# Kernel optimization log

Measured on AMD Instinct MI355X. Metric: run time of the kernel, lower is better.

Reference implementation:

```python
import jax, jax.numpy as jnp
import numpy as np

BATCH = 4096
TEMP = 0.5
WORLD = 1
B = BATCH * WORLD
N = 2 * B
DIM = 128


def _neg_indices():
    # mask_correlated_samples: ones(N,N) with diagonal and the two +/-B
    # off-diagonals zeroed; negatives are entries where mask is True.
    mask = np.ones((N, N), dtype=bool)
    np.fill_diagonal(mask, False)
    idx = np.arange(B)
    mask[idx, idx + B] = False
    mask[idx + B, idx] = False
    rows, cols = np.nonzero(mask)  # each row has exactly N-2 negatives
    return rows.reshape(N, N - 2), cols.reshape(N, N - 2)

_NEG_ROWS, _NEG_COLS = _neg_indices()


def setup_inputs() -> dict:
    key = jax.random.key(0)
    k1, k2 = jax.random.split(key)
    z_i = jax.random.normal(k1, (BATCH, DIM), dtype=jnp.float32)
    z_j = jax.random.normal(k2, (BATCH, DIM), dtype=jnp.float32)
    return {"z_i": z_i, "z_j": z_j}


def reference(z_i, z_j):
    z = jnp.concatenate([z_i, z_j], axis=0)                 # [N, D]
    z = z / jnp.linalg.norm(z, axis=1, keepdims=True)       # L2 normalize
    # cosine similarity of unit vectors == dot product
    sim = (z @ z.T) / TEMP                                   # [N, N]
    sim_i_j = jnp.diagonal(sim, offset=B)                    # [B]
    sim_j_i = jnp.diagonal(sim, offset=-B)                   # [B]
    pos = jnp.concatenate([sim_i_j, sim_j_i])[:, None]       # [N, 1]
    neg = sim[_NEG_ROWS, _NEG_COLS]                          # [N, N-2]
    logits = jnp.concatenate([pos, neg], axis=1)             # [N, N-1]
    # CrossEntropyLoss(reduction='sum') with labels all zero, then / N
    loss = jnp.sum(jax.scipy.special.logsumexp(logits, axis=1) - logits[:, 0])
    return loss / N
```

## Files before the change

kernel.cpp:

```cpp
#include <hip/hip_runtime.h>
#include <hip/hip_bf16.h>


#define NN 8192
#define BHALF 4096
#define DIMK 128

typedef __bf16 bf16x8 __attribute__((ext_vector_type(8)));
typedef float f32x4 __attribute__((ext_vector_type(4)));

#define C1F 2.8853900817779268f
#define SCALEF 1.6986436f

__global__ __launch_bounds__(256) void nt_normalize(
    const float* __restrict__ zi, const float* __restrict__ zj,
    unsigned int* __restrict__ zb_packed) {
  int row = blockIdx.x * 4 + (threadIdx.x >> 6);
  int lane = threadIdx.x & 63;
  const float* src = (row < BHALF) ? (zi + (size_t)row * DIMK)
                                   : (zj + (size_t)(row - BHALF) * DIMK);
  float2 v = ((const float2*)src)[lane];
  float ss = v.x * v.x + v.y * v.y;
#pragma unroll
  for (int off = 32; off >= 1; off >>= 1) ss += __shfl_xor(ss, off, 64);
  float rn = rsqrtf(ss) * SCALEF;
  __hip_bfloat16 h0 = __float2bfloat16(v.x * rn);
  __hip_bfloat16 h1 = __float2bfloat16(v.y * rn);
  unsigned int packed = ((unsigned int)(*(unsigned short*)&h1) << 16) |
                        (*(unsigned short*)&h0);
  int tile = row >> 4, t = row & 15;
  int cq = lane >> 2;
  int c = cq >> 2, quad = cq & 3;
  size_t widx = ((size_t)((tile * 4 + c) * 64 + quad * 16 + t)) * 4 + (lane & 3);
  zb_packed[widx] = packed;
}

__global__ __launch_bounds__(256, 2) void nt_sim(
    const uint4* __restrict__ zbv, float* __restrict__ part) {
  const int lane = threadIdx.x & 63;
  const int wave = threadIdx.x >> 6;
  const int quad = lane >> 4;
  const int t = lane & 15;
  const int row_tile0 = blockIdx.y * 16 + wave * 4;
  const int TB0 = blockIdx.x * 32;

  bf16x8 A[4][4];
#pragma unroll
  for (int rt = 0; rt < 4; ++rt)
#pragma unroll
    for (int c = 0; c < 4; ++c)
      A[rt][c] = __builtin_bit_cast(
          bf16x8, zbv[(size_t)((row_tile0 + rt) * 4 + c) * 64 + lane]);

  float sum[4][4];
#pragma unroll
  for (int rt = 0; rt < 4; ++rt)
#pragma unroll
    for (int r = 0; r < 4; ++r) sum[rt][r] = 0.f;

  uint4 nb[4];
#pragma unroll
  for (int c = 0; c < 4; ++c) nb[c] = zbv[(size_t)(TB0 * 4 + c) * 64 + lane];

  for (int ct = 0; ct < 32; ++ct) {
    uint4 cb[4];
#pragma unroll
    for (int c = 0; c < 4; ++c) cb[c] = nb[c];
#pragma unroll
    for (int c = 0; c < 4; ++c)
      nb[c] = zbv[(size_t)((TB0 + ct + 1) * 4 + c) * 64 + lane];
    f32x4 acc[4];
#pragma unroll
    for (int rt = 0; rt < 4; ++rt) acc[rt] = (f32x4){0.f, 0.f, 0.f, 0.f};
#pragma unroll
    for (int c = 0; c < 4; ++c)
#pragma unroll
      for (int rt = 0; rt < 4; ++rt)
        acc[rt] = __builtin_amdgcn_mfma_f32_16x16x32_bf16(
            A[rt][c], __builtin_bit_cast(bf16x8, cb[c]), acc[rt], 0, 0, 0);
#pragma unroll
    for (int rt = 0; rt < 4; ++rt)
#pragma unroll
      for (int r = 0; r < 4; ++r)
        sum[rt][r] += __builtin_amdgcn_exp2f(acc[rt][r]);
  }

#pragma unroll
  for (int off = 8; off >= 1; off >>= 1)
#pragma unroll
    for (int rt = 0; rt < 4; ++rt)
#pragma unroll
      for (int r = 0; r < 4; ++r)
        sum[rt][r] += __shfl_xor(sum[rt][r], off, 16);

  if (t == 0) {
    float* dst = part + (size_t)blockIdx.x * NN;
    int row_base = row_tile0 * 16;
#pragma unroll
    for (int rt = 0; rt < 4; ++rt)
#pragma unroll
      for (int r = 0; r < 4; ++r)
        dst[row_base + rt * 16 + quad * 4 + r] = sum[rt][r];
  }
}

__device__ __forceinline__ float bf2f(unsigned short s) {
  unsigned int u = (unsigned int)s << 16;
  return __builtin_bit_cast(float, u);
}

__global__ __launch_bounds__(256) void nt_finalize(
    const uint4* __restrict__ zbv, const float* __restrict__ part,
    float* __restrict__ out) {
  int i = blockIdx.x * 256 + threadIdx.x;
  int tile = i >> 4, t = i & 15;
  int p = i ^ BHALF;
  int tilep = p >> 4;
  float S = 0.f;
#pragma unroll
  for (int k = 0; k < 16; ++k) S += part[(size_t)k * NN + i];
  float dp = 0.f, dd = 0.f;
#pragma unroll
  for (int cq = 0; cq < 16; ++cq) {
    int c = cq >> 2, q = cq & 3;
    uint4 ua = zbv[(size_t)((tile * 4 + c) * 64 + q * 16 + t)];
    uint4 up = zbv[(size_t)((tilep * 4 + c) * 64 + q * 16 + t)];
    const unsigned short* pa = (const unsigned short*)&ua;
    const unsigned short* pp = (const unsigned short*)&up;
#pragma unroll
    for (int k = 0; k < 8; ++k) {
      float a = bf2f(pa[k]), pv = bf2f(pp[k]);
      dd = fmaf(a, a, dd);
      dp = fmaf(a, pv, dp);
    }
  }
  float diag = __builtin_amdgcn_exp2f(dd);
  float v = logf(S - diag) - (2.0f / C1F) * dp;
#pragma unroll
  for (int off = 32; off >= 1; off >>= 1) v += __shfl_xor(v, off, 64);
  __shared__ float wsum[4];
  if ((threadIdx.x & 63) == 0) wsum[threadIdx.x >> 6] = v;
  __syncthreads();
  if (threadIdx.x == 0)
    atomicAdd(out, (wsum[0] + wsum[1] + wsum[2] + wsum[3]) * (1.0f / (float)NN));
}

extern "C" void kernel_launch(void* const* d_in, const int* in_sizes, int n_in,
                              void* d_out, int out_size, void* d_ws,
                              size_t ws_size, hipStream_t stream) {
  const float* zi = (const float*)d_in[0];
  const float* zj = (const float*)d_in[1];

  unsigned int* zb = (unsigned int*)d_ws;
  float* part = (float*)((char*)d_ws + (size_t)NN * DIMK * 2);

  hipMemsetAsync(d_out, 0, sizeof(float), stream);

  nt_normalize<<<NN / 4, 256, 0, stream>>>(zi, zj, zb);

  dim3 grid(16, 32);
  nt_sim<<<grid, 256, 0, stream>>>((const uint4*)zb, part);

  nt_finalize<<<NN / 256, 256, 0, stream>>>((const uint4*)zb, part,
                                            (float*)d_out);
}
```

Baseline: 84.67 us.

## Split column range across more blocks, double-buffer B tiles, fold output zeroing

The similarity kernel now covers 16 column tiles per block instead of 32, which doubles the grid to 32x32 blocks, and the finalize pass sums 32 partials instead of 16. The inner loop is unrolled by two with two B register buffers so each tile's loads are issued while the other tile's MFMAs run. The launch-bounds occupancy hint rises from 2 to 3 blocks per CU. The output memset is folded into the normalize kernel to save one launch, and the partial buffer offset moves to 4 MiB. The costs are more partial-sum traffic and higher register pressure under the tighter occupancy bound.

```diff
diff --git a/kernel.cpp b/kernel.cpp
--- a/kernel.cpp
+++ b/kernel.cpp
@@ -14,7 +14,8 @@
 
 __global__ __launch_bounds__(256) void nt_normalize(
     const float* __restrict__ zi, const float* __restrict__ zj,
-    unsigned int* __restrict__ zb_packed) {
+    unsigned int* __restrict__ zb_packed, float* __restrict__ out) {
+  if (blockIdx.x == 0 && threadIdx.x == 0) out[0] = 0.0f;
   int row = blockIdx.x * 4 + (threadIdx.x >> 6);
   int lane = threadIdx.x & 63;
   const float* src = (row < BHALF) ? (zi + (size_t)row * DIMK)
@@ -35,14 +36,14 @@
   zb_packed[widx] = packed;
 }
 
-__global__ __launch_bounds__(256, 2) void nt_sim(
+__global__ __launch_bounds__(256, 3) void nt_sim(
     const uint4* __restrict__ zbv, float* __restrict__ part) {
   const int lane = threadIdx.x & 63;
   const int wave = threadIdx.x >> 6;
   const int quad = lane >> 4;
   const int t = lane & 15;
   const int row_tile0 = blockIdx.y * 16 + wave * 4;
-  const int TB0 = blockIdx.x * 32;
+  const int TB0 = blockIdx.x * 16;
 
   bf16x8 A[4][4];
 #pragma unroll
@@ -58,17 +59,15 @@
 #pragma unroll
     for (int r = 0; r < 4; ++r) sum[rt][r] = 0.f;
 
-  uint4 nb[4];
+  uint4 b0[4], b1[4];
 #pragma unroll
-  for (int c = 0; c < 4; ++c) nb[c] = zbv[(size_t)(TB0 * 4 + c) * 64 + lane];
+  for (int c = 0; c < 4; ++c)
+    b0[c] = zbv[(size_t)((TB0 + 0) * 4 + c) * 64 + lane];
+#pragma unroll
+  for (int c = 0; c < 4; ++c)
+    b1[c] = zbv[(size_t)((TB0 + 1) * 4 + c) * 64 + lane];
 
-  for (int ct = 0; ct < 32; ++ct) {
-    uint4 cb[4];
-#pragma unroll
-    for (int c = 0; c < 4; ++c) cb[c] = nb[c];
-#pragma unroll
-    for (int c = 0; c < 4; ++c)
-      nb[c] = zbv[(size_t)((TB0 + ct + 1) * 4 + c) * 64 + lane];
+  for (int ct = 0; ct < 16; ct += 2) {
     f32x4 acc[4];
 #pragma unroll
     for (int rt = 0; rt < 4; ++rt) acc[rt] = (f32x4){0.f, 0.f, 0.f, 0.f};
@@ -77,7 +76,27 @@
 #pragma unroll
       for (int rt = 0; rt < 4; ++rt)
         acc[rt] = __builtin_amdgcn_mfma_f32_16x16x32_bf16(
-            A[rt][c], __builtin_bit_cast(bf16x8, cb[c]), acc[rt], 0, 0, 0);
+            A[rt][c], __builtin_bit_cast(bf16x8, b0[c]), acc[rt], 0, 0, 0);
+#pragma unroll
+    for (int c = 0; c < 4; ++c)
+      b0[c] = zbv[(size_t)((TB0 + ct + 2) * 4 + c) * 64 + lane];
+#pragma unroll
+    for (int rt = 0; rt < 4; ++rt)
+#pragma unroll
+      for (int r = 0; r < 4; ++r)
+        sum[rt][r] += __builtin_amdgcn_exp2f(acc[rt][r]);
+
+#pragma unroll
+    for (int rt = 0; rt < 4; ++rt) acc[rt] = (f32x4){0.f, 0.f, 0.f, 0.f};
+#pragma unroll
+    for (int c = 0; c < 4; ++c)
+#pragma unroll
+      for (int rt = 0; rt < 4; ++rt)
+        acc[rt] = __builtin_amdgcn_mfma_f32_16x16x32_bf16(
+            A[rt][c], __builtin_bit_cast(bf16x8, b1[c]), acc[rt], 0, 0, 0);
+#pragma unroll
+    for (int c = 0; c < 4; ++c)
+      b1[c] = zbv[(size_t)((TB0 + ct + 3) * 4 + c) * 64 + lane];
 #pragma unroll
     for (int rt = 0; rt < 4; ++rt)
 #pragma unroll
@@ -118,7 +137,7 @@
   int tilep = p >> 4;
   float S = 0.f;
 #pragma unroll
-  for (int k = 0; k < 16; ++k) S += part[(size_t)k * NN + i];
+  for (int k = 0; k < 32; ++k) S += part[(size_t)k * NN + i];
   float dp = 0.f, dd = 0.f;
 #pragma unroll
   for (int cq = 0; cq < 16; ++cq) {
@@ -152,13 +171,11 @@
   const float* zj = (const float*)d_in[1];
 
   unsigned int* zb = (unsigned int*)d_ws;
-  float* part = (float*)((char*)d_ws + (size_t)NN * DIMK * 2);
+  float* part = (float*)((char*)d_ws + (4u << 20));
 
-  hipMemsetAsync(d_out, 0, sizeof(float), stream);
+  nt_normalize<<<NN / 4, 256, 0, stream>>>(zi, zj, zb, (float*)d_out);
 
-  nt_normalize<<<NN / 4, 256, 0, stream>>>(zi, zj, zb);
-
-  dim3 grid(16, 32);
+  dim3 grid(32, 32);
   nt_sim<<<grid, 256, 0, stream>>>((const uint4*)zb, part);
 
   nt_finalize<<<NN / 256, 256, 0, stream>>>((const uint4*)zb, part,
```

After: 137.9 us. 1.63x slower.

## Stage column tiles in LDS via global_load_lds and double the column grid

Applied to the files above, without the earlier changes.

The similarity kernel now copies its 16 column tiles (64KB) into shared memory with asynchronous global-to-LDS loads, then runs the MFMA loop from LDS instead of register-prefetched global loads. The grid's column dimension doubles to 32 blocks, each covering half as many column tiles, so finalize sums 32 partials. The output memset is folded into the normalize kernel to drop a separate launch. The 64KB of LDS per block may limit occupancy, and each block now issues a barrier before computing.

```diff
diff --git a/kernel.cpp b/kernel.cpp
--- a/kernel.cpp
+++ b/kernel.cpp
@@ -14,7 +14,8 @@
 
 __global__ __launch_bounds__(256) void nt_normalize(
     const float* __restrict__ zi, const float* __restrict__ zj,
-    unsigned int* __restrict__ zb_packed) {
+    unsigned int* __restrict__ zb_packed, float* __restrict__ out) {
+  if (blockIdx.x == 0 && threadIdx.x == 0) out[0] = 0.0f;
   int row = blockIdx.x * 4 + (threadIdx.x >> 6);
   int lane = threadIdx.x & 63;
   const float* src = (row < BHALF) ? (zi + (size_t)row * DIMK)
@@ -37,12 +38,27 @@
 
 __global__ __launch_bounds__(256, 2) void nt_sim(
     const uint4* __restrict__ zbv, float* __restrict__ part) {
+  __shared__ uint4 ldsb[4096];
+
   const int lane = threadIdx.x & 63;
   const int wave = threadIdx.x >> 6;
   const int quad = lane >> 4;
   const int t = lane & 15;
   const int row_tile0 = blockIdx.y * 16 + wave * 4;
-  const int TB0 = blockIdx.x * 32;
+
+  {
+    const char* gsrc = (const char*)zbv + (size_t)blockIdx.x * 65536;
+#pragma unroll
+    for (int k = 0; k < 16; ++k) {
+      int chunk = k * 4 + wave;
+      __builtin_amdgcn_global_load_lds(
+          (const __attribute__((address_space(1))) unsigned int*)(
+              gsrc + chunk * 1024 + lane * 16),
+          (__attribute__((address_space(3))) unsigned int*)(
+              (char*)ldsb + chunk * 1024),
+          16, 0, 0);
+    }
+  }
 
   bf16x8 A[4][4];
 #pragma unroll
@@ -58,26 +74,21 @@
 #pragma unroll
     for (int r = 0; r < 4; ++r) sum[rt][r] = 0.f;
 
-  uint4 nb[4];
-#pragma unroll
-  for (int c = 0; c < 4; ++c) nb[c] = zbv[(size_t)(TB0 * 4 + c) * 64 + lane];
+  __syncthreads();
 
-  for (int ct = 0; ct < 32; ++ct) {
-    uint4 cb[4];
-#pragma unroll
-    for (int c = 0; c < 4; ++c) cb[c] = nb[c];
-#pragma unroll
-    for (int c = 0; c < 4; ++c)
-      nb[c] = zbv[(size_t)((TB0 + ct + 1) * 4 + c) * 64 + lane];
+#pragma unroll 2
+  for (int ct = 0; ct < 16; ++ct) {
     f32x4 acc[4];
 #pragma unroll
     for (int rt = 0; rt < 4; ++rt) acc[rt] = (f32x4){0.f, 0.f, 0.f, 0.f};
 #pragma unroll
-    for (int c = 0; c < 4; ++c)
+    for (int c = 0; c < 4; ++c) {
+      bf16x8 bv = __builtin_bit_cast(bf16x8, ldsb[(ct * 4 + c) * 64 + lane]);
 #pragma unroll
       for (int rt = 0; rt < 4; ++rt)
-        acc[rt] = __builtin_amdgcn_mfma_f32_16x16x32_bf16(
-            A[rt][c], __builtin_bit_cast(bf16x8, cb[c]), acc[rt], 0, 0, 0);
+        acc[rt] = __builtin_amdgcn_mfma_f32_16x16x32_bf16(A[rt][c], bv,
+                                                          acc[rt], 0, 0, 0);
+    }
 #pragma unroll
     for (int rt = 0; rt < 4; ++rt)
 #pragma unroll
@@ -118,7 +129,7 @@
   int tilep = p >> 4;
   float S = 0.f;
 #pragma unroll
-  for (int k = 0; k < 16; ++k) S += part[(size_t)k * NN + i];
+  for (int k = 0; k < 32; ++k) S += part[(size_t)k * NN + i];
   float dp = 0.f, dd = 0.f;
 #pragma unroll
   for (int cq = 0; cq < 16; ++cq) {
@@ -152,13 +163,11 @@
   const float* zj = (const float*)d_in[1];
 
   unsigned int* zb = (unsigned int*)d_ws;
-  float* part = (float*)((char*)d_ws + (size_t)NN * DIMK * 2);
+  float* part = (float*)((char*)d_ws + (2u << 20));
 
-  hipMemsetAsync(d_out, 0, sizeof(float), stream);
+  nt_normalize<<<NN / 4, 256, 0, stream>>>(zi, zj, zb, (float*)d_out);
 
-  nt_normalize<<<NN / 4, 256, 0, stream>>>(zi, zj, zb);
-
-  dim3 grid(16, 32);
+  dim3 grid(32, 32);
   nt_sim<<<grid, 256, 0, stream>>>((const uint4*)zb, part);
 
   nt_finalize<<<NN / 256, 256, 0, stream>>>((const uint4*)zb, part,
```

Result: faster. 80.82 us (-4.5%).
